# Performance work log

Measured on AMD Instinct MI355X. Metric: run time of the kernel, lower is better.

The kernel has to match this reference:

```python
import jax, jax.numpy as jnp
import numpy as np

B, T, C = 4, 2048, 1024


def setup_inputs() -> dict:
    key = jax.random.key(0)
    ks = jax.random.split(key, 4)
    s = 1.0 / np.sqrt(C)  # ~torch Linear init scale
    return {
        "x": jax.random.normal(ks[0], (B, T, C), jnp.float32),
        "Wk": jax.random.normal(ks[1], (C, C), jnp.float32) * s,
        "Wq": jax.random.normal(ks[2], (C, C), jnp.float32) * s,
        "Wv": jax.random.normal(ks[3], (C, C), jnp.float32) * s,
        "bk": jnp.zeros((C,), jnp.float32),
        "bq": jnp.zeros((C,), jnp.float32),
        "bv": jnp.zeros((C,), jnp.float32),
    }


def reference(x, Wk, Wq, Wv, bk, bq, bv):
    # torch Linear: y = x @ W^T + b, W has shape (out, in)
    K = jnp.einsum('btc,oc->bto', x, Wk) + bk
    Q = jnp.einsum('btc,oc->bto', x, Wq) + bq
    V = jnp.einsum('btc,oc->bto', x, Wv) + bv
    c = x.shape[-1]
    # NOTE: original computes K @ Q^T (not Q @ K^T); reproduce faithfully.
    scores = jnp.einsum('btd,bsd->bts', K, Q) / jnp.sqrt(jnp.asarray(c, x.dtype))
    t = x.shape[1]
    causal = jnp.tril(jnp.ones((t, t), dtype=bool))  # [T, T]
    scores = jnp.where(causal[None, :, :], scores, -jnp.inf)
    attn = jax.nn.softmax(scores, axis=-1)  # [B, T, T]
    return jnp.einsum('bts,bsc->btc', attn, V)
```

## Files before the change

### kernel.cpp

```cpp
#include <hip/hip_runtime.h>

typedef __bf16 bf16x8 __attribute__((ext_vector_type(8)));
typedef __bf16 bf16x4v __attribute__((ext_vector_type(4)));
typedef float f32x4 __attribute__((ext_vector_type(4)));

typedef const void __attribute__((address_space(1)))* gas_ptr;
typedef void __attribute__((address_space(3)))* las_ptr;

__device__ __forceinline__ void gload16(const __bf16* g, __bf16* lds) {
  __builtin_amdgcn_global_load_lds((gas_ptr)g, (las_ptr)lds, 16, 0, 0);
}

__global__ __launch_bounds__(256) void cast_all(
    const float* __restrict__ x, const float* __restrict__ w0,
    const float* __restrict__ w1, const float* __restrict__ w2,
    __bf16* __restrict__ out) {
  int i = blockIdx.x * 256 + threadIdx.x;
  const float* src;
  int off;
  if (i < 2097152) {
    src = x; off = i;
  } else {
    int j = i - 2097152;
    int seg = j >> 18;
    off = j & 262143;
    src = (seg == 0) ? w0 : (seg == 1) ? w1 : w2;
  }
  float4 v = ((const float4*)src)[off];
  bf16x4v o = { (__bf16)v.x, (__bf16)v.y, (__bf16)v.z, (__bf16)v.w };
  ((bf16x4v*)out)[i] = o;
}

__global__ void transpose_k(const __bf16* __restrict__ V, __bf16* __restrict__ Vt,
                            int T, int C) {
  __shared__ __bf16 tile[64][68];
  int b = blockIdx.z;
  int s0 = blockIdx.x * 64, c0 = blockIdx.y * 64;
  const __bf16* Vb = V + (size_t)b * T * C;
  __bf16* Vtb = Vt + (size_t)b * C * T;
  const int t = threadIdx.x;
  const int sr = t >> 3, e8 = (t & 7) * 8;
#pragma unroll
  for (int it = 0; it < 2; ++it) {
    int s = it * 32 + sr;
    bf16x8 v = *(const bf16x8*)&Vb[(size_t)(s0 + s) * C + c0 + e8];
#pragma unroll
    for (int j = 0; j < 8; ++j) tile[s][e8 + j] = v[j];
  }
  __syncthreads();
#pragma unroll
  for (int it = 0; it < 2; ++it) {
    int c = it * 32 + sr;
    bf16x8 o;
#pragma unroll
    for (int j = 0; j < 8; ++j) o[j] = tile[e8 + j][c];
    *(bf16x8*)&Vtb[(size_t)(c0 + c) * T + s0 + e8] = o;
  }
}

__global__ __launch_bounds__(256) void rowsum_k(const __bf16* __restrict__ E,
                                                float* __restrict__ rinv, int T) {
  const int row = blockIdx.x;
  const int t = row & (T - 1);
  const int wlim = ((t >> 7) + 1) << 7;
  const __bf16* er = E + (size_t)row * T;
  const int tid = threadIdx.x, lane = tid & 63, wave = tid >> 6;
  __shared__ float red[4];
  float s = 0.f;
  if (tid * 8 < wlim) {
    bf16x8 v = ((const bf16x8*)er)[tid];
#pragma unroll
    for (int j = 0; j < 8; ++j) s += (float)v[j];
  }
#pragma unroll
  for (int off = 32; off; off >>= 1) s += __shfl_down(s, off);
  if (lane == 0) red[wave] = s;
  __syncthreads();
  if (tid == 0) rinv[row] = 1.f / (red[0] + red[1] + red[2] + red[3]);
}

template <int MODE>
__global__ __launch_bounds__(256) void gemm_nt(
    const __bf16* __restrict__ A, const __bf16* __restrict__ B, void* __restrict__ Out,
    int lda, int ldb, int ldo, int nkt_full,
    const float* __restrict__ bias0, const float* __restrict__ bias1,
    const float* __restrict__ bias2, float scale, const float* __restrict__ rinv_g,
    size_t strideA_z, size_t strideB_z, size_t strideO_z) {
  if (MODE == 1 && blockIdx.y > blockIdx.x) return;
  const int z = blockIdx.z;
  A += (size_t)z * strideA_z;
  B += (size_t)z * strideB_z;
  const int m0 = blockIdx.x * 128;
  const int n0 = blockIdx.y * 128;
  int nkt = nkt_full;
  if (MODE == 2) nkt = min(nkt, (int)(blockIdx.x + 1) * 4);

  __shared__ __align__(16) __bf16 smA[2][128 * 32];
  __shared__ __align__(16) __bf16 smB[2][128 * 32];

  const int tid = threadIdx.x;
  const int lane = tid & 63;
  const int wave = tid >> 6;
  const int grow = lane >> 2;
  const int gcol = ((lane & 3) ^ ((lane >> 3) & 3)) << 3;

  const __bf16* Ab = A + (size_t)m0 * lda;
  const __bf16* Bb = B + (size_t)n0 * ldb;

  auto stage = [&](int buf, int kt) {
    const int kofs = kt * 32 + gcol;
#pragma unroll
    for (int rr = 0; rr < 2; ++rr) {
      int br = rr * 64 + wave * 16;
      gload16(Ab + (size_t)(br + grow) * lda + kofs, &smA[buf][br * 32]);
      gload16(Bb + (size_t)(br + grow) * ldb + kofs, &smB[buf][br * 32]);
    }
  };

  f32x4 acc[4][4];
  const f32x4 zero = {0.f, 0.f, 0.f, 0.f};
#pragma unroll
  for (int m = 0; m < 4; ++m)
#pragma unroll
    for (int n = 0; n < 4; ++n) acc[m][n] = zero;

  const int wr = (wave >> 1) * 64;
  const int wc = (wave & 1) * 64;
  const int lr = lane & 15;
  const int kg = lane >> 4;
  const int phys = (kg ^ ((lr >> 1) & 3)) << 3;

  stage(0, 0);
  __syncthreads();
  int cur = 0;
  for (int kt = 0; kt < nkt; ++kt) {
    if (kt + 1 < nkt) stage(cur ^ 1, kt + 1);
    bf16x8 af[4], bfr[4];
#pragma unroll
    for (int m = 0; m < 4; ++m)
      af[m] = *(const bf16x8*)&smA[cur][(wr + m * 16 + lr) * 32 + phys];
#pragma unroll
    for (int n = 0; n < 4; ++n)
      bfr[n] = *(const bf16x8*)&smB[cur][(wc + n * 16 + lr) * 32 + phys];
#pragma unroll
    for (int m = 0; m < 4; ++m)
#pragma unroll
      for (int n = 0; n < 4; ++n)
        acc[m][n] = __builtin_amdgcn_mfma_f32_16x16x32_bf16(af[m], bfr[n], acc[m][n], 0, 0, 0);
    __syncthreads();
    cur ^= 1;
  }

#pragma unroll
  for (int m = 0; m < 4; ++m) {
#pragma unroll
    for (int i = 0; i < 4; ++i) {
      int r = m0 + wr + m * 16 + kg * 4 + i;
      float ri = (MODE == 2) ? rinv_g[z * 2048 + r] : 0.f;
#pragma unroll
      for (int n = 0; n < 4; ++n) {
        int c = n0 + wc + n * 16 + lr;
        float v = acc[m][n][i];
        if (MODE == 0) {
          const float* bias = (z == 0) ? bias0 : (z == 1) ? bias1 : bias2;
          ((__bf16*)Out)[(size_t)z * strideO_z + (size_t)r * ldo + c] = (__bf16)(v + bias[c]);
        } else if (MODE == 1) {
          float e = (c <= r) ? __expf(v * scale - 8.0f) : 0.0f;
          ((__bf16*)Out)[(size_t)z * strideO_z + (size_t)r * ldo + c] = (__bf16)e;
        } else {
          ((float*)Out)[(size_t)z * strideO_z + (size_t)r * ldo + c] = v * ri;
        }
      }
    }
  }
}

extern "C" void kernel_launch(void* const* d_in, const int* in_sizes, int n_in,
                              void* d_out, int out_size, void* d_ws, size_t ws_size,
                              hipStream_t stream) {
  const float* x  = (const float*)d_in[0];
  const float* Wk = (const float*)d_in[1];
  const float* Wq = (const float*)d_in[2];
  const float* Wv = (const float*)d_in[3];
  const float* bk = (const float*)d_in[4];
  const float* bq = (const float*)d_in[5];
  const float* bv = (const float*)d_in[6];
  float* out = (float*)d_out;

  const int B = 4, T = 2048, C = 1024;
  const int M = B * T;

  char* ws = (char*)d_ws;
  __bf16* x_bf = (__bf16*)ws;
  __bf16* w_bf = (__bf16*)(ws + 16777216);
  __bf16* kqv  = (__bf16*)(ws + 23068672);
  __bf16* vt   = (__bf16*)(ws + 73400320);
  __bf16* E    = (__bf16*)(ws + 90177536);
  float*  rinv = (float*)(ws + 123731968);

  cast_all<<<11264, 256, 0, stream>>>(x, Wk, Wq, Wv, x_bf);

  gemm_nt<0><<<dim3(M / 128, C / 128, 3), 256, 0, stream>>>(
      x_bf, w_bf, kqv, C, C, C, C / 32, bk, bq, bv, 1.f, nullptr,
      (size_t)0, (size_t)C * C, (size_t)M * C);

  transpose_k<<<dim3(T / 64, C / 64, B), 256, 0, stream>>>(
      kqv + 2 * (size_t)M * C, vt, T, C);

  gemm_nt<1><<<dim3(T / 128, T / 128, B), 256, 0, stream>>>(
      kqv, kqv + (size_t)M * C, E, C, C, T, C / 32, nullptr, nullptr, nullptr,
      0.03125f, nullptr, (size_t)T * C, (size_t)T * C, (size_t)T * T);

  rowsum_k<<<B * T, 256, 0, stream>>>(E, rinv, T);

  gemm_nt<2><<<dim3(T / 128, C / 128, B), 256, 0, stream>>>(
      E, vt, out, T, T, C, T / 32, nullptr, nullptr, nullptr, 1.f, rinv,
      (size_t)T * T, (size_t)C * T, (size_t)T * C);
}
```

Before: 190.5 us.

## Fuse softmax row sums into score GEMM and remap causal grids

The separate row-sum kernel is removed. The score GEMM epilogue now reduces exp values per row across lanes and atomically adds them into a zeroed buffer. The score GEMM uses a compact triangular block index instead of launching and early-exiting upper-triangle blocks. The PV GEMM uses a 1D grid that schedules longer causal rows first for better load balance. These changes add atomics, a memset, and sqrt-based index decoding, and row sums now come from fp32 values rather than rounded bf16.

```diff
diff --git a/kernel.cpp b/kernel.cpp
--- a/kernel.cpp
+++ b/kernel.cpp
@@ -58,42 +58,38 @@
   }
 }
 
-__global__ __launch_bounds__(256) void rowsum_k(const __bf16* __restrict__ E,
-                                                float* __restrict__ rinv, int T) {
-  const int row = blockIdx.x;
-  const int t = row & (T - 1);
-  const int wlim = ((t >> 7) + 1) << 7;
-  const __bf16* er = E + (size_t)row * T;
-  const int tid = threadIdx.x, lane = tid & 63, wave = tid >> 6;
-  __shared__ float red[4];
-  float s = 0.f;
-  if (tid * 8 < wlim) {
-    bf16x8 v = ((const bf16x8*)er)[tid];
-#pragma unroll
-    for (int j = 0; j < 8; ++j) s += (float)v[j];
-  }
-#pragma unroll
-  for (int off = 32; off; off >>= 1) s += __shfl_down(s, off);
-  if (lane == 0) red[wave] = s;
-  __syncthreads();
-  if (tid == 0) rinv[row] = 1.f / (red[0] + red[1] + red[2] + red[3]);
-}
-
 template <int MODE>
 __global__ __launch_bounds__(256) void gemm_nt(
     const __bf16* __restrict__ A, const __bf16* __restrict__ B, void* __restrict__ Out,
     int lda, int ldb, int ldo, int nkt_full,
     const float* __restrict__ bias0, const float* __restrict__ bias1,
-    const float* __restrict__ bias2, float scale, const float* __restrict__ rinv_g,
+    const float* __restrict__ bias2, float scale, float* __restrict__ rsum,
     size_t strideA_z, size_t strideB_z, size_t strideO_z) {
-  if (MODE == 1 && blockIdx.y > blockIdx.x) return;
-  const int z = blockIdx.z;
+  int bx, by, z;
+  if (MODE == 0) {
+    bx = blockIdx.x; by = blockIdx.y; z = blockIdx.z;
+  } else if (MODE == 1) {
+    int f = blockIdx.x;
+    z = f & 3;
+    int t = f >> 2;
+    bx = (int)((sqrtf(8.f * (float)t + 1.f) - 1.f) * 0.5f);
+    while ((bx + 1) * (bx + 2) / 2 <= t) ++bx;
+    while (bx * (bx + 1) / 2 > t) --bx;
+    by = t - bx * (bx + 1) / 2;
+  } else {
+    int f = blockIdx.x;
+    int half = f >> 8, idx = f & 255;
+    int rem = idx & 31;
+    by = rem >> 2; z = rem & 3;
+    int bh = idx >> 5;
+    bx = half ? bh : 15 - bh;
+  }
   A += (size_t)z * strideA_z;
   B += (size_t)z * strideB_z;
-  const int m0 = blockIdx.x * 128;
-  const int n0 = blockIdx.y * 128;
+  const int m0 = bx * 128;
+  const int n0 = by * 128;
   int nkt = nkt_full;
-  if (MODE == 2) nkt = min(nkt, (int)(blockIdx.x + 1) * 4);
+  if (MODE == 2) nkt = min(nkt, (bx + 1) * 4);
 
   __shared__ __align__(16) __bf16 smA[2][128 * 32];
   __shared__ __align__(16) __bf16 smB[2][128 * 32];
@@ -156,7 +152,8 @@
 #pragma unroll
     for (int i = 0; i < 4; ++i) {
       int r = m0 + wr + m * 16 + kg * 4 + i;
-      float ri = (MODE == 2) ? rinv_g[z * 2048 + r] : 0.f;
+      float ri = (MODE == 2) ? 1.0f / rsum[z * 2048 + r] : 0.f;
+      float rs = 0.f;
 #pragma unroll
       for (int n = 0; n < 4; ++n) {
         int c = n0 + wc + n * 16 + lr;
@@ -167,9 +164,15 @@
         } else if (MODE == 1) {
           float e = (c <= r) ? __expf(v * scale - 8.0f) : 0.0f;
           ((__bf16*)Out)[(size_t)z * strideO_z + (size_t)r * ldo + c] = (__bf16)e;
+          rs += e;
         } else {
           ((float*)Out)[(size_t)z * strideO_z + (size_t)r * ldo + c] = v * ri;
         }
+      }
+      if (MODE == 1) {
+#pragma unroll
+        for (int off = 1; off < 16; off <<= 1) rs += __shfl_xor(rs, off);
+        if (lr == 0) atomicAdd(&rsum[z * 2048 + r], rs);
       }
     }
   }
@@ -196,9 +199,11 @@
   __bf16* kqv  = (__bf16*)(ws + 23068672);
   __bf16* vt   = (__bf16*)(ws + 73400320);
   __bf16* E    = (__bf16*)(ws + 90177536);
-  float*  rinv = (float*)(ws + 123731968);
+  float*  rsum = (float*)(ws + 123731968);
 
   cast_all<<<11264, 256, 0, stream>>>(x, Wk, Wq, Wv, x_bf);
+
+  hipMemsetAsync(rsum, 0, (size_t)M * sizeof(float), stream);
 
   gemm_nt<0><<<dim3(M / 128, C / 128, 3), 256, 0, stream>>>(
       x_bf, w_bf, kqv, C, C, C, C / 32, bk, bq, bv, 1.f, nullptr,
@@ -207,13 +212,11 @@
   transpose_k<<<dim3(T / 64, C / 64, B), 256, 0, stream>>>(
       kqv + 2 * (size_t)M * C, vt, T, C);
 
-  gemm_nt<1><<<dim3(T / 128, T / 128, B), 256, 0, stream>>>(
+  gemm_nt<1><<<dim3(544), 256, 0, stream>>>(
       kqv, kqv + (size_t)M * C, E, C, C, T, C / 32, nullptr, nullptr, nullptr,
-      0.03125f, nullptr, (size_t)T * C, (size_t)T * C, (size_t)T * T);
-
-  rowsum_k<<<B * T, 256, 0, stream>>>(E, rinv, T);
-
-  gemm_nt<2><<<dim3(T / 128, C / 128, B), 256, 0, stream>>>(
-      E, vt, out, T, T, C, T / 32, nullptr, nullptr, nullptr, 1.f, rinv,
+      0.03125f, rsum, (size_t)T * C, (size_t)T * C, (size_t)T * T);
+
+  gemm_nt<2><<<dim3(512), 256, 0, stream>>>(
+      E, vt, out, T, T, C, T / 32, nullptr, nullptr, nullptr, 1.f, rsum,
       (size_t)T * T, (size_t)C * T, (size_t)T * C);
 }
```

Measured after the change: 159.3 us (median of 2 runs). 16.4% less time.
